# Performance work log

Hardware: AMD Instinct MI355X
Metric: run time of the kernel (lower is better)

Reference implementation:

```python
import jax, jax.numpy as jnp
import numpy as np
import math

B, S, H = 8, 4096, 1024
E, I, K = 8, 2048, 2
CAP_FACTOR = 1.0


def setup_inputs() -> dict:
    key = jax.random.key(0)
    k1, k2, k3, k4 = jax.random.split(key, 4)
    # kaiming_uniform (linear): bound = sqrt(3 / fan_in), fan_in = last dim
    def kaiming(k, shape):
        bound = math.sqrt(3.0 / shape[-1])
        return jax.random.uniform(k, shape, jnp.float32, -bound, bound)
    x = jax.random.normal(k1, (B, S, H), jnp.float32)
    expert_embeddings = kaiming(k2, (E, H))
    first_linear = kaiming(k3, (E, I, H))
    second_linear = kaiming(k4, (E, H, I))
    return {"x": x, "expert_embeddings": expert_embeddings,
            "first_linear": first_linear, "second_linear": second_linear}


def _router(x, expert_embeddings):
    # dot: [B, S, E]
    dot = jnp.einsum('bsh,eh->bse', x, expert_embeddings)
    n = dot.shape[0] * dot.shape[1]
    dot2 = dot.reshape(n, E)
    vals, idx = jax.lax.top_k(dot2, K)                       # [N, K]
    rows = jnp.arange(n)[:, None]
    masked = jnp.full_like(dot2, -jnp.inf).at[rows, idx].set(vals)
    return jax.nn.softmax(masked, axis=-1)                   # [N, E]


def reference(x, expert_embeddings, first_linear, second_linear):
    batch, seq, hidden = x.shape
    n_tokens = batch * seq
    expert_capacity = math.ceil(n_tokens / E * CAP_FACTOR)

    weights = _router(x, expert_embeddings)                  # [N, E]
    ones = (weights > 0).astype(weights.dtype)               # tokens routed to expert
    # capacity mask: keep first expert_capacity tokens (in token order) per expert
    cap_ones = jnp.where(jnp.cumsum(ones, axis=0) <= expert_capacity, ones, 0.0)
    caw = weights * cap_ones                                 # [N, E]

    # topk over token dim per expert -> selected token slots
    vals, idx = jax.lax.top_k(caw.T, expert_capacity)        # [E, C]
    index = idx.reshape(-1)                                  # [E*C]

    x_flat = x.reshape(n_tokens, hidden)
    tokens = x_flat[index].reshape(E, expert_capacity, hidden)   # gather

    inter = jax.nn.relu(jnp.einsum('ech,eih->eci', tokens, first_linear))
    out = jnp.einsum('eci,ehi->ech', inter, second_linear)
    out = out * vals[:, :, None]                             # weight by router prob

    final = jnp.zeros((n_tokens, hidden), x.dtype).at[index].add(
        out.reshape(-1, hidden))                             # scatter-add combine
    return final.reshape(x.shape)
```

## Files before the change

### kernel.cpp

```cpp
#include <hip/hip_runtime.h>
#include <stdint.h>

#define N_TOK 32768
#define HID   1024
#define NE    8
#define NI    2048
#define CAP   4096

typedef short s16x8 __attribute__((ext_vector_type(8)));
typedef float f32x4 __attribute__((ext_vector_type(4)));

__device__ __forceinline__ unsigned short f2bf(float f) {
    unsigned int u = __builtin_bit_cast(unsigned int, f);
    u += 0x7fffu + ((u >> 16) & 1u);
    return (unsigned short)(u >> 16);
}

__device__ __forceinline__ void gload16(const void* g, void* l) {
    __builtin_amdgcn_global_load_lds(
        (const __attribute__((address_space(1))) unsigned int*)(uintptr_t)g,
        (__attribute__((address_space(3))) unsigned int*)(unsigned int)(uintptr_t)l,
        16, 0, 0);
}

#define WAIT_LGKM0 asm volatile("s_waitcnt lgkmcnt(0)" ::: "memory")
#define WAIT_VM4   asm volatile("s_waitcnt vmcnt(4)" ::: "memory")
#define WAIT_VM0   asm volatile("s_waitcnt vmcnt(0)" ::: "memory")
#define SFENCE     __builtin_amdgcn_sched_barrier(0)
#define BARR       __builtin_amdgcn_s_barrier()

#define STG(DST, SRC, H, TT) do { \
    unsigned short* _d = (DST) + (H) * 8192 + wave * 1024; \
    gload16(SRC[H][0] + (size_t)(TT) * 64 + gsl8, _d); \
    gload16(SRC[H][1] + (size_t)(TT) * 64 + gsl8, _d + 512); } while (0)

#define RD_A(BASE, MH) do { \
    _Pragma("unroll") for (int m2 = 0; m2 < 4; ++m2) \
    _Pragma("unroll") for (int ks = 0; ks < 2; ++ks) \
        afr[m2*2+ks] = *(const s16x8*)((BASE) + aoff + (MH)*4096 + m2*1024 + phs[ks]); } while (0)

#define RD_B(BF, BASE, NH) do { \
    _Pragma("unroll") for (int n2 = 0; n2 < 2; ++n2) \
    _Pragma("unroll") for (int ks = 0; ks < 2; ++ks) \
        BF[n2*2+ks] = *(const s16x8*)((BASE) + boff + (NH)*2048 + n2*1024 + phs[ks]); } while (0)

#define MFMA_Q(MH, NH, BF) do { \
    __builtin_amdgcn_s_setprio(1); \
    _Pragma("unroll") for (int m2 = 0; m2 < 4; ++m2) \
    _Pragma("unroll") for (int n2 = 0; n2 < 2; ++n2) \
    _Pragma("unroll") for (int ks = 0; ks < 2; ++ks) \
        acc[(MH)*4+m2][(NH)*2+n2] = __builtin_amdgcn_mfma_f32_16x16x32_bf16( \
            afr[m2*2+ks], BF[n2*2+ks], acc[(MH)*4+m2][(NH)*2+n2], 0, 0, 0); \
    __builtin_amdgcn_s_setprio(0); } while (0)

#define KLOOP8(T) \
    for (int it = 0; it < (T) / 2; ++it) { \
        const int t0 = 2 * it, t1 = t0 + 1; \
        const bool lastI = (it == (T) / 2 - 1); \
         \
        STG(Abuf1, rA, 1, t1); \
        RD_A(Abuf0, 0); RD_B(bfr0, Bbuf0, 0); \
        SFENCE; BARR; WAIT_LGKM0; SFENCE; \
        MFMA_Q(0, 0, bfr0); BARR; SFENCE; \
         \
        STG(Bbuf1, rB, 1, t1); \
        RD_B(bfr1, Bbuf0, 1); \
        SFENCE; BARR; WAIT_LGKM0; SFENCE; \
        MFMA_Q(0, 1, bfr1); BARR; SFENCE; \
         \
        if (t0 + 2 < (T)) STG(Bbuf0, rB, 0, t0 + 2); \
        RD_A(Abuf0, 1); \
        SFENCE; BARR; WAIT_LGKM0; SFENCE; \
        MFMA_Q(1, 0, bfr0); BARR; SFENCE; \
         \
        if (t0 + 2 < (T)) STG(Bbuf0, rB, 1, t0 + 2); \
        if (lastI) { WAIT_VM0; } else { WAIT_VM4; } \
        SFENCE; BARR; SFENCE; \
        MFMA_Q(1, 1, bfr1); BARR; SFENCE; \
         \
        if (t0 + 2 < (T)) STG(Abuf0, rA, 0, t0 + 2); \
        RD_A(Abuf1, 0); RD_B(bfr0, Bbuf1, 0); \
        SFENCE; BARR; WAIT_LGKM0; SFENCE; \
        MFMA_Q(0, 0, bfr0); BARR; SFENCE; \
         \
        if (t0 + 2 < (T)) STG(Abuf0, rA, 1, t0 + 2); \
        RD_B(bfr1, Bbuf1, 1); \
        SFENCE; BARR; WAIT_LGKM0; SFENCE; \
        MFMA_Q(0, 1, bfr1); BARR; SFENCE; \
         \
        if (t1 + 2 < (T)) STG(Bbuf1, rB, 0, t1 + 2); \
        RD_A(Abuf1, 1); \
        SFENCE; BARR; WAIT_LGKM0; SFENCE; \
        MFMA_Q(1, 0, bfr0); BARR; SFENCE; \
         \
        if (t1 + 2 < (T)) STG(Abuf1, rA, 0, t1 + 2); \
        if (lastI) { WAIT_VM0; } else { WAIT_VM4; } \
        SFENCE; BARR; SFENCE; \
        MFMA_Q(1, 1, bfr1); BARR; SFENCE; \
    }

#define KPROLOGUE \
    STG(Abuf0, rA, 0, 0); STG(Abuf0, rA, 1, 0); \
    STG(Bbuf0, rB, 0, 0); STG(Bbuf0, rB, 1, 0); \
    STG(Bbuf1, rB, 0, 1); STG(Abuf1, rA, 0, 1); \
    WAIT_VM4; SFENCE; BARR; SFENCE;

__global__ __launch_bounds__(256) void cvt_kernel(
    const float* __restrict__ src, unsigned short* __restrict__ dst, size_t n8)
{
    size_t i = (size_t)blockIdx.x * 256 + threadIdx.x;
    size_t stride = (size_t)gridDim.x * 256;
    for (; i < n8; i += stride) {
        float4 a0 = ((const float4*)src)[2 * i];
        float4 a1 = ((const float4*)src)[2 * i + 1];
        uint4 p;
        p.x = f2bf(a0.x) | ((unsigned)f2bf(a0.y) << 16);
        p.y = f2bf(a0.z) | ((unsigned)f2bf(a0.w) << 16);
        p.z = f2bf(a1.x) | ((unsigned)f2bf(a1.y) << 16);
        p.w = f2bf(a1.z) | ((unsigned)f2bf(a1.w) << 16);
        ((uint4*)dst)[i] = p;
    }
}

__global__ __launch_bounds__(256) void router_kernel(
    const float* __restrict__ x, const float* __restrict__ emb,
    int2* __restrict__ r_e, float2* __restrict__ r_w,
    unsigned short* __restrict__ xb)
{
    int token = blockIdx.x * 4 + (threadIdx.x >> 6);
    int lane  = threadIdx.x & 63;
    const float4* xr = (const float4*)(x + (size_t)token * HID);
    const float4* er = (const float4*)emb;

    float a[NE];
#pragma unroll
    for (int e = 0; e < NE; ++e) a[e] = 0.f;
    uint2 pk[4];
#pragma unroll
    for (int j = 0; j < 4; ++j) {
        float4 v = xr[j * 64 + lane];
        pk[j].x = f2bf(v.x) | ((unsigned)f2bf(v.y) << 16);
        pk[j].y = f2bf(v.z) | ((unsigned)f2bf(v.w) << 16);
#pragma unroll
        for (int e = 0; e < NE; ++e) {
            float4 w = er[e * 256 + j * 64 + lane];
            a[e] += v.x * w.x + v.y * w.y + v.z * w.z + v.w * w.w;
        }
    }
    uint2* xbr = (uint2*)(xb + (size_t)token * HID);
#pragma unroll
    for (int j = 0; j < 4; ++j) xbr[j * 64 + lane] = pk[j];

#pragma unroll
    for (int e = 0; e < NE; ++e) {
        for (int off = 32; off; off >>= 1) a[e] += __shfl_xor(a[e], off);
    }
    if (lane == 0) {
        float v1 = -1e30f, v2 = -1e30f; int i1 = 0, i2 = 0;
#pragma unroll
        for (int e = 0; e < NE; ++e) {
            float v = a[e];
            if (v > v1) { v2 = v1; i2 = i1; v1 = v; i1 = e; }
            else if (v > v2) { v2 = v; i2 = e; }
        }
        float ex = __expf(v2 - v1);
        r_e[token] = make_int2(i1, i2);
        r_w[token] = make_float2(1.f / (1.f + ex), ex / (1.f + ex));
    }
}

__global__ __launch_bounds__(1024) void count_kernel(
    const int2* __restrict__ r_e, int* __restrict__ bc)
{
    __shared__ int cnt[NE];
    if (threadIdx.x < NE) cnt[threadIdx.x] = 0;
    __syncthreads();
    int n = blockIdx.x * 1024 + threadIdx.x;
    int2 e = r_e[n];
    atomicAdd(&cnt[e.x], 1);
    atomicAdd(&cnt[e.y], 1);
    __syncthreads();
    if (threadIdx.x < NE) bc[blockIdx.x * NE + threadIdx.x] = cnt[threadIdx.x];
}

__global__ void prefix_kernel(const int* __restrict__ bc, int* __restrict__ bb)
{
    int e = threadIdx.x;
    if (e >= NE) return;
    int run = 0;
    for (int b = 0; b < N_TOK / 1024; ++b) {
        bb[b * NE + e] = run;
        run += bc[b * NE + e];
    }
}

__global__ __launch_bounds__(1024) void assign_kernel(
    const int2* __restrict__ r_e, const float2* __restrict__ r_w,
    const int* __restrict__ bb,
    int* __restrict__ tok_list, float* __restrict__ w_list)
{
    __shared__ int wavecnt[16][NE];
    __shared__ int waveoff[16][NE];
    int tid = threadIdx.x, lane = tid & 63, wv = tid >> 6;
    int n = blockIdx.x * 1024 + tid;
    int2 e = r_e[n];
    float2 w = r_w[n];
    unsigned long long below = (1ull << lane) - 1ull;
    int rank0 = 0, rank1 = 0;
#pragma unroll
    for (int ex = 0; ex < NE; ++ex) {
        unsigned long long m = __ballot(e.x == ex || e.y == ex);
        if (lane == 0) wavecnt[wv][ex] = __popcll(m);
        int r = __popcll(m & below);
        if (e.x == ex) rank0 = r;
        if (e.y == ex) rank1 = r;
    }
    __syncthreads();
    if (tid < NE) {
        int run = 0;
        for (int w2 = 0; w2 < 16; ++w2) { waveoff[w2][tid] = run; run += wavecnt[w2][tid]; }
    }
    __syncthreads();
    int s0 = bb[blockIdx.x * NE + e.x] + waveoff[wv][e.x] + rank0;
    int s1 = bb[blockIdx.x * NE + e.y] + waveoff[wv][e.y] + rank1;
    if (s0 < CAP) { tok_list[e.x * CAP + s0] = n; w_list[e.x * CAP + s0] = w.x; }
    if (s1 < CAP) { tok_list[e.y * CAP + s1] = n; w_list[e.y * CAP + s1] = w.y; }
}


__global__ __launch_bounds__(512, 2) void gemm1_k(
    const unsigned short* __restrict__ xb,
    const unsigned short* __restrict__ w1b,
    const int* __restrict__ tok_list,
    unsigned short* __restrict__ inter,
    int eb)
{
    constexpr int K = HID, T = K / 64;
    __shared__ __align__(16) unsigned short smem[65536];
    unsigned short* const Abuf0 = smem;
    unsigned short* const Bbuf0 = smem + 16384;
    unsigned short* const Abuf1 = smem + 32768;
    unsigned short* const Bbuf1 = smem + 49152;

    const int nblk = gridDim.x;
    const int lin  = blockIdx.x;
    const int wg   = (lin & 7) * (nblk >> 3) + (lin >> 3);
    const int tn = wg & 7;
    const int tm = (wg >> 3) & 15;
    const int ez = wg >> 7;
    const int e  = eb + ez;

    const int tid = threadIdx.x, lane = tid & 63, wave = tid >> 6;
    const int wr = wave >> 2, wc = wave & 3;
    const int gsl8 = ((lane & 7) ^ ((lane >> 3) & 7)) * 8;
    const int aoff = (wr * 128 + (lane & 15)) * 64;
    const int boff = (wc * 64 + (lane & 15)) * 64;
    const int phs[2] = { (((lane >> 4)) ^ (lane & 7)) * 8,
                         ((4 + (lane >> 4)) ^ (lane & 7)) * 8 };

    const int* tl = tok_list + e * CAP + tm * 256;
    const unsigned short* rA[2][2];
    const unsigned short* rB[2][2];
#pragma unroll
    for (int h = 0; h < 2; ++h)
#pragma unroll
        for (int j = 0; j < 2; ++j) {
            int row = h * 128 + wave * 16 + (lane >> 3) + j * 8;
            rA[h][j] = xb + (size_t)tl[row] * K;
            rB[h][j] = w1b + ((size_t)e * NI + tn * 256 + row) * K;
        }

    f32x4 acc[8][4];
#pragma unroll
    for (int i = 0; i < 8; ++i)
#pragma unroll
        for (int j = 0; j < 4; ++j) acc[i][j] = (f32x4)0.f;

    s16x8 afr[8], bfr0[4], bfr1[4];

    KPROLOGUE
#pragma unroll 1
    KLOOP8(T)

    __syncthreads();
#pragma unroll
    for (int mi = 0; mi < 8; ++mi)
#pragma unroll
        for (int ni = 0; ni < 4; ++ni)
#pragma unroll
            for (int r = 0; r < 4; ++r) {
                int row = wr * 128 + mi * 16 + (lane >> 4) * 4 + r;
                int c   = wc * 64 + ni * 16 + (lane & 15);
                float v = acc[mi][ni][r];
                v = v > 0.f ? v : 0.f;
                smem[row * 256 + (((c >> 3) ^ (row & 7)) << 3) + (c & 7)] = f2bf(v);
            }
    __syncthreads();
    unsigned short* Cp = inter + ((size_t)ez * CAP + tm * 256) * NI + tn * 256;
#pragma unroll
    for (int itv = 0; itv < 16; ++itv) {
        int v = tid + itv * 512;
        int row = v >> 5, s = v & 31;
        uint4 val = *(const uint4*)&smem[row * 256 + ((s ^ (row & 7)) << 3)];
        *(uint4*)&Cp[(size_t)row * NI + s * 8] = val;
    }
}

__global__ __launch_bounds__(512, 2) void gemm2_k(
    const unsigned short* __restrict__ inter,
    const unsigned short* __restrict__ w2b,
    const int* __restrict__ tok_list,
    const float* __restrict__ w_list,
    float* __restrict__ out,
    int eb)
{
    constexpr int K = NI, T = K / 64;
    __shared__ __align__(16) unsigned short smem[65536];
    unsigned short* const Abuf0 = smem;
    unsigned short* const Bbuf0 = smem + 16384;
    unsigned short* const Abuf1 = smem + 32768;
    unsigned short* const Bbuf1 = smem + 49152;

    const int nblk = gridDim.x;
    const int lin  = blockIdx.x;
    const int wg   = (lin & 7) * (nblk >> 3) + (lin >> 3);
    const int tn = wg & 3;
    const int tm = (wg >> 2) & 15;
    const int ez = wg >> 6;
    const int e  = eb + ez;

    const int tid = threadIdx.x, lane = tid & 63, wave = tid >> 6;
    const int wr = wave >> 2, wc = wave & 3;
    const int gsl8 = ((lane & 7) ^ ((lane >> 3) & 7)) * 8;
    const int aoff = (wr * 128 + (lane & 15)) * 64;
    const int boff = (wc * 64 + (lane & 15)) * 64;
    const int phs[2] = { (((lane >> 4)) ^ (lane & 7)) * 8,
                         ((4 + (lane >> 4)) ^ (lane & 7)) * 8 };

    const unsigned short* rA[2][2];
    const unsigned short* rB[2][2];
#pragma unroll
    for (int h = 0; h < 2; ++h)
#pragma unroll
        for (int j = 0; j < 2; ++j) {
            int row = h * 128 + wave * 16 + (lane >> 3) + j * 8;
            rA[h][j] = inter + ((size_t)ez * CAP + tm * 256 + row) * (size_t)K;
            rB[h][j] = w2b + ((size_t)e * HID + tn * 256 + row) * (size_t)K;
        }

    f32x4 acc[8][4];
#pragma unroll
    for (int i = 0; i < 8; ++i)
#pragma unroll
        for (int j = 0; j < 4; ++j) acc[i][j] = (f32x4)0.f;

    s16x8 afr[8], bfr0[4], bfr1[4];

    KPROLOGUE
#pragma unroll 1
    KLOOP8(T)

    const int* tl   = tok_list + e * CAP + tm * 256;
    const float* wl = w_list  + e * CAP + tm * 256;
#pragma unroll
    for (int mi = 0; mi < 8; ++mi)
#pragma unroll
        for (int r = 0; r < 4; ++r) {
            int rrow = wr * 128 + mi * 16 + (lane >> 4) * 4 + r;
            int tok  = tl[rrow];
            float w  = wl[rrow];
            float* orow = out + (size_t)tok * HID + tn * 256 + wc * 64;
#pragma unroll
            for (int ni = 0; ni < 4; ++ni)
                atomicAdd(&orow[ni * 16 + (lane & 15)], acc[mi][ni][r] * w);
        }
}

extern "C" void kernel_launch(void* const* d_in, const int* in_sizes, int n_in,
                              void* d_out, int out_size, void* d_ws, size_t ws_size,
                              hipStream_t stream)
{
    const float* x   = (const float*)d_in[0];
    const float* emb = (const float*)d_in[1];
    const float* W1  = (const float*)d_in[2];
    const float* W2  = (const float*)d_in[3];
    float* out = (float*)d_out;

    size_t off = 0;
    auto alloc = [&](size_t bytes) -> void* {
        void* p = (char*)d_ws + off;
        off += (bytes + 255) & ~(size_t)255;
        return p;
    };
    const size_t sz_w  = (size_t)NE * NI * HID * 2;
    const size_t sz_xb = (size_t)N_TOK * HID * 2;

    int*   tok_list = (int*)alloc((size_t)NE * CAP * 4);
    float* w_list   = (float*)alloc((size_t)NE * CAP * 4);
    unsigned short* w1b = (unsigned short*)alloc(sz_w);
    unsigned short* w2b = (unsigned short*)alloc(sz_w);
    unsigned short* xb  = (unsigned short*)alloc(sz_xb);

    unsigned short* inter = (unsigned short*)((char*)d_ws + off);
    size_t avail = ws_size > off ? ws_size - off : 0;
    const size_t per_e = (size_t)CAP * NI * 2;
    int G = (avail >= 8 * per_e) ? 8 : (avail >= 4 * per_e) ? 4
          : (avail >= 2 * per_e) ? 2 : 1;

    int2*   r_e = (int2*)inter;
    float2* r_w = (float2*)((char*)inter + (size_t)N_TOK * 8);
    int*    bc  = (int*)((char*)inter + (size_t)N_TOK * 16);
    int*    bb  = bc + (N_TOK / 1024) * NE;

    hipMemsetAsync(d_out, 0, (size_t)N_TOK * HID * 4, stream);
    hipMemsetAsync(tok_list, 0, (size_t)NE * CAP * 4, stream);
    hipMemsetAsync(w_list, 0, (size_t)NE * CAP * 4, stream);

    cvt_kernel<<<2048, 256, 0, stream>>>(W1, w1b, (size_t)NE * NI * HID / 8);
    cvt_kernel<<<2048, 256, 0, stream>>>(W2, w2b, (size_t)NE * HID * NI / 8);
    router_kernel<<<N_TOK / 4, 256, 0, stream>>>(x, emb, r_e, r_w, xb);
    count_kernel<<<N_TOK / 1024, 1024, 0, stream>>>(r_e, bc);
    prefix_kernel<<<1, 64, 0, stream>>>(bc, bb);
    assign_kernel<<<N_TOK / 1024, 1024, 0, stream>>>(r_e, r_w, bb, tok_list, w_list);

    for (int eb = 0; eb < NE; eb += G) {
        gemm1_k<<<dim3(8 * 16 * G), 512, 0, stream>>>(xb, w1b, tok_list, inter, eb);
        gemm2_k<<<dim3(4 * 16 * G), 512, 0, stream>>>(inter, w2b, tok_list, w_list, out, eb);
    }
}
```

Baseline: 478.9 us.

## Restage GEMM K-loop prefetch, fuse weight conversion, replace atomic scatter with combine kernel

Reorganizes the GEMM K-loop so each buffer half loads all four tile chunks at once with a deeper vmcnt wait, and removes a __syncthreads after gemm1's loop. Merges the two weight-conversion launches into one kernel. When all experts fit in the workspace, gemm2 writes bf16 expert outputs through swizzled LDS into a staging buffer (reusing the xb buffer). A new combine kernel then gathers the up to two weighted contributions per token and writes the output without atomics, which also removes the output memset. This trades fp32 atomics for an extra bf16 round-trip and rounding of expert outputs, and reusing xb assumes gemm1 has finished reading it.

```diff
diff --git a/kernel.cpp b/kernel.cpp
--- a/kernel.cpp
+++ b/kernel.cpp
@@ -16,6 +16,10 @@
     return (unsigned short)(u >> 16);
 }
 
+__device__ __forceinline__ float bf2f(unsigned short u) {
+    return __builtin_bit_cast(float, (unsigned int)u << 16);
+}
+
 __device__ __forceinline__ void gload16(const void* g, void* l) {
     __builtin_amdgcn_global_load_lds(
         (const __attribute__((address_space(1))) unsigned int*)(uintptr_t)g,
@@ -24,15 +28,16 @@
 }
 
 #define WAIT_LGKM0 asm volatile("s_waitcnt lgkmcnt(0)" ::: "memory")
-#define WAIT_VM4   asm volatile("s_waitcnt vmcnt(4)" ::: "memory")
+#define WAIT_VM8   asm volatile("s_waitcnt vmcnt(8)" ::: "memory")
 #define WAIT_VM0   asm volatile("s_waitcnt vmcnt(0)" ::: "memory")
 #define SFENCE     __builtin_amdgcn_sched_barrier(0)
 #define BARR       __builtin_amdgcn_s_barrier()
 
-#define STG(DST, SRC, H, TT) do { \
-    unsigned short* _d = (DST) + (H) * 8192 + wave * 1024; \
-    gload16(SRC[H][0] + (size_t)(TT) * 64 + gsl8, _d); \
-    gload16(SRC[H][1] + (size_t)(TT) * 64 + gsl8, _d + 512); } while (0)
+#define STG_T(DST, SRC, TT) do { \
+    gload16(SRC[0][0] + (size_t)(TT) * 64 + gsl8, (DST) + wave * 1024); \
+    gload16(SRC[0][1] + (size_t)(TT) * 64 + gsl8, (DST) + wave * 1024 + 512); \
+    gload16(SRC[1][0] + (size_t)(TT) * 64 + gsl8, (DST) + 8192 + wave * 1024); \
+    gload16(SRC[1][1] + (size_t)(TT) * 64 + gsl8, (DST) + 8192 + wave * 1024 + 512); } while (0)
 
 #define RD_A(BASE, MH) do { \
     _Pragma("unroll") for (int m2 = 0; m2 < 4; ++m2) \
@@ -55,70 +60,62 @@
 
 #define KLOOP8(T) \
     for (int it = 0; it < (T) / 2; ++it) { \
-        const int t0 = 2 * it, t1 = t0 + 1; \
-        const bool lastI = (it == (T) / 2 - 1); \
-         \
-        STG(Abuf1, rA, 1, t1); \
+        const int t0 = 2 * it; \
+        const int tp2 = (t0 + 2 < (T)) ? t0 + 2 : (T) - 1; \
+        const int tp3 = (t0 + 3 < (T)) ? t0 + 3 : (T) - 1; \
+         \
         RD_A(Abuf0, 0); RD_B(bfr0, Bbuf0, 0); \
-        SFENCE; BARR; WAIT_LGKM0; SFENCE; \
-        MFMA_Q(0, 0, bfr0); BARR; SFENCE; \
-         \
-        STG(Bbuf1, rB, 1, t1); \
+        SFENCE; BARR; WAIT_LGKM0; SFENCE; MFMA_Q(0, 0, bfr0); BARR; SFENCE; \
+         \
         RD_B(bfr1, Bbuf0, 1); \
-        SFENCE; BARR; WAIT_LGKM0; SFENCE; \
-        MFMA_Q(0, 1, bfr1); BARR; SFENCE; \
-         \
-        if (t0 + 2 < (T)) STG(Bbuf0, rB, 0, t0 + 2); \
+        SFENCE; BARR; WAIT_LGKM0; SFENCE; MFMA_Q(0, 1, bfr1); BARR; SFENCE; \
+         \
+        STG_T(Bbuf0, rB, tp2); \
         RD_A(Abuf0, 1); \
-        SFENCE; BARR; WAIT_LGKM0; SFENCE; \
-        MFMA_Q(1, 0, bfr0); BARR; SFENCE; \
-         \
-        if (t0 + 2 < (T)) STG(Bbuf0, rB, 1, t0 + 2); \
-        if (lastI) { WAIT_VM0; } else { WAIT_VM4; } \
-        SFENCE; BARR; SFENCE; \
-        MFMA_Q(1, 1, bfr1); BARR; SFENCE; \
-         \
-        if (t0 + 2 < (T)) STG(Abuf0, rA, 0, t0 + 2); \
+        SFENCE; BARR; WAIT_LGKM0; SFENCE; MFMA_Q(1, 0, bfr0); BARR; SFENCE; \
+         \
+        STG_T(Abuf0, rA, tp2); \
+        SFENCE; BARR; SFENCE; MFMA_Q(1, 1, bfr1); WAIT_VM8; SFENCE; BARR; SFENCE; \
+         \
         RD_A(Abuf1, 0); RD_B(bfr0, Bbuf1, 0); \
-        SFENCE; BARR; WAIT_LGKM0; SFENCE; \
-        MFMA_Q(0, 0, bfr0); BARR; SFENCE; \
-         \
-        if (t0 + 2 < (T)) STG(Abuf0, rA, 1, t0 + 2); \
+        SFENCE; BARR; WAIT_LGKM0; SFENCE; MFMA_Q(0, 0, bfr0); BARR; SFENCE; \
+         \
         RD_B(bfr1, Bbuf1, 1); \
-        SFENCE; BARR; WAIT_LGKM0; SFENCE; \
-        MFMA_Q(0, 1, bfr1); BARR; SFENCE; \
-         \
-        if (t1 + 2 < (T)) STG(Bbuf1, rB, 0, t1 + 2); \
+        SFENCE; BARR; WAIT_LGKM0; SFENCE; MFMA_Q(0, 1, bfr1); BARR; SFENCE; \
+         \
+        STG_T(Bbuf1, rB, tp3); \
         RD_A(Abuf1, 1); \
-        SFENCE; BARR; WAIT_LGKM0; SFENCE; \
-        MFMA_Q(1, 0, bfr0); BARR; SFENCE; \
-         \
-        if (t1 + 2 < (T)) STG(Abuf1, rA, 0, t1 + 2); \
-        if (lastI) { WAIT_VM0; } else { WAIT_VM4; } \
-        SFENCE; BARR; SFENCE; \
-        MFMA_Q(1, 1, bfr1); BARR; SFENCE; \
-    }
+        SFENCE; BARR; WAIT_LGKM0; SFENCE; MFMA_Q(1, 0, bfr0); BARR; SFENCE; \
+         \
+        STG_T(Abuf1, rA, tp3); \
+        SFENCE; BARR; SFENCE; MFMA_Q(1, 1, bfr1); WAIT_VM8; SFENCE; BARR; SFENCE; \
+    } \
+    WAIT_VM0; SFENCE; BARR; SFENCE;
 
 #define KPROLOGUE \
-    STG(Abuf0, rA, 0, 0); STG(Abuf0, rA, 1, 0); \
-    STG(Bbuf0, rB, 0, 0); STG(Bbuf0, rB, 1, 0); \
-    STG(Bbuf1, rB, 0, 1); STG(Abuf1, rA, 0, 1); \
-    WAIT_VM4; SFENCE; BARR; SFENCE;
-
-__global__ __launch_bounds__(256) void cvt_kernel(
-    const float* __restrict__ src, unsigned short* __restrict__ dst, size_t n8)
+    STG_T(Bbuf0, rB, 0); STG_T(Abuf0, rA, 0); \
+    STG_T(Bbuf1, rB, 1); STG_T(Abuf1, rA, 1); \
+    WAIT_VM8; SFENCE; BARR; SFENCE;
+
+__global__ __launch_bounds__(256) void cvt2_kernel(
+    const float* __restrict__ s1, unsigned short* __restrict__ d1, size_t n81,
+    const float* __restrict__ s2, unsigned short* __restrict__ d2, size_t n82)
 {
     size_t i = (size_t)blockIdx.x * 256 + threadIdx.x;
     size_t stride = (size_t)gridDim.x * 256;
-    for (; i < n8; i += stride) {
-        float4 a0 = ((const float4*)src)[2 * i];
-        float4 a1 = ((const float4*)src)[2 * i + 1];
+    size_t total = n81 + n82;
+    for (; i < total; i += stride) {
+        const float* src; unsigned short* dst; size_t j;
+        if (i < n81) { src = s1; dst = d1; j = i; }
+        else         { src = s2; dst = d2; j = i - n81; }
+        float4 a0 = ((const float4*)src)[2 * j];
+        float4 a1 = ((const float4*)src)[2 * j + 1];
         uint4 p;
         p.x = f2bf(a0.x) | ((unsigned)f2bf(a0.y) << 16);
         p.y = f2bf(a0.z) | ((unsigned)f2bf(a0.w) << 16);
         p.z = f2bf(a1.x) | ((unsigned)f2bf(a1.y) << 16);
         p.w = f2bf(a1.z) | ((unsigned)f2bf(a1.w) << 16);
-        ((uint4*)dst)[i] = p;
+        ((uint4*)dst)[j] = p;
     }
 }
 
@@ -197,7 +194,8 @@
 __global__ __launch_bounds__(1024) void assign_kernel(
     const int2* __restrict__ r_e, const float2* __restrict__ r_w,
     const int* __restrict__ bb,
-    int* __restrict__ tok_list, float* __restrict__ w_list)
+    int* __restrict__ tok_list, float* __restrict__ w_list,
+    int2* __restrict__ smap)
 {
     __shared__ int wavecnt[16][NE];
     __shared__ int waveoff[16][NE];
@@ -223,8 +221,41 @@
     __syncthreads();
     int s0 = bb[blockIdx.x * NE + e.x] + waveoff[wv][e.x] + rank0;
     int s1 = bb[blockIdx.x * NE + e.y] + waveoff[wv][e.y] + rank1;
-    if (s0 < CAP) { tok_list[e.x * CAP + s0] = n; w_list[e.x * CAP + s0] = w.x; }
-    if (s1 < CAP) { tok_list[e.y * CAP + s1] = n; w_list[e.y * CAP + s1] = w.y; }
+    int g0 = -1, g1 = -1;
+    if (s0 < CAP) { tok_list[e.x * CAP + s0] = n; w_list[e.x * CAP + s0] = w.x; g0 = e.x * CAP + s0; }
+    if (s1 < CAP) { tok_list[e.y * CAP + s1] = n; w_list[e.y * CAP + s1] = w.y; g1 = e.y * CAP + s1; }
+    smap[n] = make_int2(g0, g1);
+}
+
+__global__ __launch_bounds__(256) void combine_kernel(
+    const unsigned short* __restrict__ out_e,
+    const int2* __restrict__ smap,
+    const float* __restrict__ w_list,
+    float* __restrict__ out)
+{
+    int t  = blockIdx.x * 2 + (threadIdx.x >> 7);
+    int h0 = (threadIdx.x & 127) * 8;
+    int2 s = smap[t];
+    float r[8];
+#pragma unroll
+    for (int i = 0; i < 8; ++i) r[i] = 0.f;
+    if (s.x >= 0) {
+        float w = w_list[s.x];
+        uint4 v = *(const uint4*)(out_e + (size_t)s.x * HID + h0);
+        const unsigned short* pv = (const unsigned short*)&v;
+#pragma unroll
+        for (int i = 0; i < 8; ++i) r[i] += w * bf2f(pv[i]);
+    }
+    if (s.y >= 0) {
+        float w = w_list[s.y];
+        uint4 v = *(const uint4*)(out_e + (size_t)s.y * HID + h0);
+        const unsigned short* pv = (const unsigned short*)&v;
+#pragma unroll
+        for (int i = 0; i < 8; ++i) r[i] += w * bf2f(pv[i]);
+    }
+    float4* o = (float4*)(out + (size_t)t * HID + h0);
+    o[0] = make_float4(r[0], r[1], r[2], r[3]);
+    o[1] = make_float4(r[4], r[5], r[6], r[7]);
 }
 
 
@@ -282,7 +313,6 @@
 #pragma unroll 1
     KLOOP8(T)
 
-    __syncthreads();
 #pragma unroll
     for (int mi = 0; mi < 8; ++mi)
 #pragma unroll
@@ -312,6 +342,7 @@
     const int* __restrict__ tok_list,
     const float* __restrict__ w_list,
     float* __restrict__ out,
+    unsigned short* __restrict__ out_e,
     int eb)
 {
     constexpr int K = NI, T = K / 64;
@@ -360,20 +391,42 @@
 #pragma unroll 1
     KLOOP8(T)
 
-    const int* tl   = tok_list + e * CAP + tm * 256;
-    const float* wl = w_list  + e * CAP + tm * 256;
-#pragma unroll
-    for (int mi = 0; mi < 8; ++mi)
-#pragma unroll
-        for (int r = 0; r < 4; ++r) {
-            int rrow = wr * 128 + mi * 16 + (lane >> 4) * 4 + r;
-            int tok  = tl[rrow];
-            float w  = wl[rrow];
-            float* orow = out + (size_t)tok * HID + tn * 256 + wc * 64;
+    if (out_e) {
+#pragma unroll
+        for (int mi = 0; mi < 8; ++mi)
 #pragma unroll
             for (int ni = 0; ni < 4; ++ni)
-                atomicAdd(&orow[ni * 16 + (lane & 15)], acc[mi][ni][r] * w);
+#pragma unroll
+                for (int r = 0; r < 4; ++r) {
+                    int row = wr * 128 + mi * 16 + (lane >> 4) * 4 + r;
+                    int c   = wc * 64 + ni * 16 + (lane & 15);
+                    smem[row * 256 + (((c >> 3) ^ (row & 7)) << 3) + (c & 7)] = f2bf(acc[mi][ni][r]);
+                }
+        __syncthreads();
+        unsigned short* Cp = out_e + ((size_t)e * CAP + tm * 256) * HID + tn * 256;
+#pragma unroll
+        for (int itv = 0; itv < 16; ++itv) {
+            int v = tid + itv * 512;
+            int row = v >> 5, s = v & 31;
+            uint4 val = *(const uint4*)&smem[row * 256 + ((s ^ (row & 7)) << 3)];
+            *(uint4*)&Cp[(size_t)row * HID + s * 8] = val;
         }
+    } else {
+        const int* tl   = tok_list + e * CAP + tm * 256;
+        const float* wl = w_list  + e * CAP + tm * 256;
+#pragma unroll
+        for (int mi = 0; mi < 8; ++mi)
+#pragma unroll
+            for (int r = 0; r < 4; ++r) {
+                int rrow = wr * 128 + mi * 16 + (lane >> 4) * 4 + r;
+                int tok  = tl[rrow];
+                float w  = wl[rrow];
+                float* orow = out + (size_t)tok * HID + tn * 256 + wc * 64;
+#pragma unroll
+                for (int ni = 0; ni < 4; ++ni)
+                    atomicAdd(&orow[ni * 16 + (lane & 15)], acc[mi][ni][r] * w);
+            }
+    }
 }
 
 extern "C" void kernel_launch(void* const* d_in, const int* in_sizes, int n_in,
@@ -397,6 +450,7 @@
 
     int*   tok_list = (int*)alloc((size_t)NE * CAP * 4);
     float* w_list   = (float*)alloc((size_t)NE * CAP * 4);
+    int2*  smap     = (int2*)alloc((size_t)N_TOK * 8);
     unsigned short* w1b = (unsigned short*)alloc(sz_w);
     unsigned short* w2b = (unsigned short*)alloc(sz_w);
     unsigned short* xb  = (unsigned short*)alloc(sz_xb);
@@ -406,25 +460,30 @@
     const size_t per_e = (size_t)CAP * NI * 2;
     int G = (avail >= 8 * per_e) ? 8 : (avail >= 4 * per_e) ? 4
           : (avail >= 2 * per_e) ? 2 : 1;
+    const bool combine = (G == 8);
+    unsigned short* out_e = combine ? xb : nullptr;
 
     int2*   r_e = (int2*)inter;
     float2* r_w = (float2*)((char*)inter + (size_t)N_TOK * 8);
     int*    bc  = (int*)((char*)inter + (size_t)N_TOK * 16);
     int*    bb  = bc + (N_TOK / 1024) * NE;
 
-    hipMemsetAsync(d_out, 0, (size_t)N_TOK * HID * 4, stream);
+    if (!combine)
+        hipMemsetAsync(d_out, 0, (size_t)N_TOK * HID * 4, stream);
     hipMemsetAsync(tok_list, 0, (size_t)NE * CAP * 4, stream);
     hipMemsetAsync(w_list, 0, (size_t)NE * CAP * 4, stream);
 
-    cvt_kernel<<<2048, 256, 0, stream>>>(W1, w1b, (size_t)NE * NI * HID / 8);
-    cvt_kernel<<<2048, 256, 0, stream>>>(W2, w2b, (size_t)NE * HID * NI / 8);
+    cvt2_kernel<<<2048, 256, 0, stream>>>(W1, w1b, (size_t)NE * NI * HID / 8,
+                                          W2, w2b, (size_t)NE * HID * NI / 8);
     router_kernel<<<N_TOK / 4, 256, 0, stream>>>(x, emb, r_e, r_w, xb);
     count_kernel<<<N_TOK / 1024, 1024, 0, stream>>>(r_e, bc);
     prefix_kernel<<<1, 64, 0, stream>>>(bc, bb);
-    assign_kernel<<<N_TOK / 1024, 1024, 0, stream>>>(r_e, r_w, bb, tok_list, w_list);
+    assign_kernel<<<N_TOK / 1024, 1024, 0, stream>>>(r_e, r_w, bb, tok_list, w_list, smap);
 
     for (int eb = 0; eb < NE; eb += G) {
         gemm1_k<<<dim3(8 * 16 * G), 512, 0, stream>>>(xb, w1b, tok_list, inter, eb);
-        gemm2_k<<<dim3(4 * 16 * G), 512, 0, stream>>>(inter, w2b, tok_list, w_list, out, eb);
-    }
-}
+        gemm2_k<<<dim3(4 * 16 * G), 512, 0, stream>>>(inter, w2b, tok_list, w_list, out, out_e, eb);
+    }
+    if (combine)
+        combine_kernel<<<N_TOK / 2, 256, 0, stream>>>(out_e, smap, w_list, out);
+}
```

Result: faster. 427.5 us (-10.7%).
